# Performance work log

Hardware: AMD Instinct MI355X
Metric: run time of the kernel (lower is better)

Reference implementation:

```python
import jax, jax.numpy as jnp
import numpy as np

N = 12  # qubits; PennyLane wire 0 = most-significant bit of the state index


def _apply_ry(state, w, theta):
    # state: [B, 2^N] complex64; theta: scalar or [B]
    B = state.shape[0]
    st = state.reshape(B, 1 << w, 2, 1 << (N - 1 - w))
    h = jnp.asarray(theta) * 0.5
    c = jnp.cos(h).reshape(-1, 1, 1)
    s = jnp.sin(h).reshape(-1, 1, 1)
    a0, a1 = st[:, :, 0, :], st[:, :, 1, :]
    st = jnp.stack([c * a0 - s * a1, s * a0 + c * a1], axis=2)
    return st.reshape(B, -1)


def _apply_rz(state, w, theta):
    B = state.shape[0]
    st = state.reshape(B, 1 << w, 2, 1 << (N - 1 - w))
    ph = jnp.exp(-0.5j * jnp.asarray(theta)).reshape(-1, 1, 1)
    a0, a1 = st[:, :, 0, :], st[:, :, 1, :]
    st = jnp.stack([ph * a0, jnp.conj(ph) * a1], axis=2)
    return st.reshape(B, -1)


def _apply_cnot(state, c, t):
    B = state.shape[0]
    st = state.reshape((B,) + (2,) * N)
    ca, ta = c + 1, t + 1
    s0 = jnp.take(st, 0, axis=ca)
    s1 = jnp.take(st, 1, axis=ca)
    s1 = jnp.flip(s1, axis=ta if ta < ca else ta - 1)  # X on target when control=1
    st = jnp.stack([s0, s1], axis=ca)
    return st.reshape(B, -1)


def _rot_layer(state, ry, rz=None):
    for q in range(N):
        state = _apply_ry(state, q, ry[q])
        if rz is not None:
            state = _apply_rz(state, q, rz[q])
    return state


def _circuit(inputs, weights):
    # inputs: [B,3] (BW, COMED, dose); weights: [108] = 9 layers x 12 qubits
    B = inputs.shape[0]
    W = weights.reshape(9, N)  # l2_ry,l2_rz,l5_ry,l5_rz,l7_ry,l7_rz,l9_ry,l9_rz,l10_ry
    state = jnp.zeros((B, 1 << N), dtype=jnp.complex64).at[:, 0].set(1.0)
    for w in range(3):                      # feature encoding
        state = _apply_ry(state, w, inputs[:, w])
    state = _rot_layer(state, W[0], W[1])   # layer 2
    for c in range(3):                      # initial -> PK entanglement
        for t in range(3, 8):
            state = _apply_cnot(state, c, t)
    for c in range(3):                      # initial -> PD entanglement
        for t in range(8, 12):
            state = _apply_cnot(state, c, t)
    state = _rot_layer(state, W[2], W[3])   # layer 5
    pk = list(range(3, 8))
    for i in range(5):                      # PK ring
        state = _apply_cnot(state, pk[i], pk[(i + 1) % 5])
    pd = list(range(8, 12))
    for i in range(4):                      # PD ring
        state = _apply_cnot(state, pd[i], pd[(i + 1) % 4])
    state = _rot_layer(state, W[4], W[5])   # layer 7
    for c, t in [(3, 8), (4, 9), (5, 10), (6, 11), (7, 8)]:  # PK-PD cross
        state = _apply_cnot(state, c, t)
    state = _rot_layer(state, W[6], W[7])   # layer 9
    state = _rot_layer(state, W[8], None)   # layer 10 (RY only)
    # <Z_q> for q = 3..11
    probs = (state.real ** 2 + state.imag ** 2).reshape((B,) + (2,) * N)
    evs = []
    for q in range(3, 12):
        p = jnp.moveaxis(probs, q + 1, -1).reshape(B, -1, 2)
        evs.append(p[:, :, 0].sum(axis=1) - p[:, :, 1].sum(axis=1))
    return jnp.stack(evs, axis=1)  # [B, 9]


def _map_to_bounds(e, bounds):
    norm = (e + 1.0) * 0.5
    lo, hi = bounds[:, 0][None, :], bounds[:, 1][None, :]
    return lo + norm * (hi - lo)


def setup_inputs() -> dict:
    key = jax.random.key(0)
    k1, k2, k3, k4 = jax.random.split(key, 4)
    B = 4096
    return {
        "subject_ids": jax.random.randint(k1, (B,), 0, 1000),
        "covariates": jax.random.normal(k2, (B, 2), dtype=jnp.float32),
        "dose_intensities": jax.random.normal(k3, (B,), dtype=jnp.float32),
        "weights": jax.random.normal(k4, (108,), dtype=jnp.float32) * 0.1,
        "pk_bounds": jnp.array([[0.5, 5.0], [2.0, 20.0], [20.0, 100.0], [2.0, 30.0], [40.0, 200.0]], dtype=jnp.float32),
        "pd_bounds": jnp.array([[5.0, 25.0], [0.3, 3.0], [0.3, 0.95], [1.0, 15.0]], dtype=jnp.float32),
    }


def reference(subject_ids, covariates, dose_intensities, weights, pk_bounds, pd_bounds):
    inputs = jnp.concatenate([covariates, dose_intensities[:, None]], axis=1)  # [B,3]
    raw = _circuit(inputs, weights)
    pk_params = _map_to_bounds(raw[:, :5], pk_bounds)
    pd_params = _map_to_bounds(raw[:, 5:], pd_bounds)
    return (pk_params, pd_params)
```

## Files before the change

### kernel.cpp

```cpp
#include <hip/hip_runtime.h>


typedef float2 cplx;
__device__ inline cplx cmul(cplx a, cplx b) {
  return make_float2(a.x * b.x - a.y * b.y, a.x * b.y + a.y * b.x);
}
__device__ inline cplx cshfl_xor(cplx v, int m) {
  return make_float2(__shfl_xor(v.x, m, 64), __shfl_xor(v.y, m, 64));
}

template <int BP>
__device__ inline void rot_gate(cplx (&a)[8], float c, float s, float cz,
                                float sz) {
  if constexpr (BP < 3) {
    constexpr int m = 1 << BP;
#pragma unroll
    for (int r = 0; r < 8; r++)
      if (!(r & m)) {
        const int r1 = r | m;
        const cplx a0 = a[r], a1 = a[r1];
        const float n0x = c * a0.x - s * a1.x, n0y = c * a0.y - s * a1.y;
        const float n1x = s * a0.x + c * a1.x, n1y = s * a0.y + c * a1.y;
        a[r] = make_float2(cz * n0x + sz * n0y, cz * n0y - sz * n0x);
        a[r1] = make_float2(cz * n1x - sz * n1y, cz * n1y + sz * n1x);
      }
  } else {
    constexpr int lm = 1 << (BP - 3);
    const int bit = (threadIdx.x >> (BP - 3)) & 1;
    const float sy = bit ? s : -s;
    const float so = bit ? -sz : sz;
#pragma unroll
    for (int r = 0; r < 8; r++) {
      const cplx p = cshfl_xor(a[r], lm);
      const float nx = c * a[r].x + sy * p.x, ny = c * a[r].y + sy * p.y;
      a[r] = make_float2(cz * nx + so * ny, cz * ny - so * nx);
    }
  }
}

template <int BP>
__device__ inline void su2_gate(cplx (&a)[8], cplx u00, cplx u01, cplx u10,
                                cplx u11) {
  if constexpr (BP < 3) {
    constexpr int m = 1 << BP;
#pragma unroll
    for (int r = 0; r < 8; r++)
      if (!(r & m)) {
        const int r1 = r | m;
        const cplx a0 = a[r], a1 = a[r1];
        const cplx t0 = cmul(u00, a0), t1 = cmul(u01, a1);
        const cplx t2 = cmul(u10, a0), t3 = cmul(u11, a1);
        a[r] = make_float2(t0.x + t1.x, t0.y + t1.y);
        a[r1] = make_float2(t2.x + t3.x, t2.y + t3.y);
      }
  } else {
    constexpr int lm = 1 << (BP - 3);
    const int bit = (threadIdx.x >> (BP - 3)) & 1;
    const cplx uA = bit ? u11 : u00;
    const cplx uB = bit ? u10 : u01;
#pragma unroll
    for (int r = 0; r < 8; r++) {
      const cplx p = cshfl_xor(a[r], lm);
      const cplx t0 = cmul(uA, a[r]), t1 = cmul(uB, p);
      a[r] = make_float2(t0.x + t1.x, t0.y + t1.y);
    }
  }
}

template <int CB, int TB>
__device__ inline void cnot_rr(cplx (&a)[8]) {
#pragma unroll
  for (int r = 0; r < 8; r++)
    if ((r & (1 << CB)) && !(r & (1 << TB))) {
      const int r1 = r | (1 << TB);
      const cplx t = a[r];
      a[r] = a[r1];
      a[r1] = t;
    }
}
template <int CB, int TL>
__device__ inline void cnot_rl(cplx (&a)[8]) {
#pragma unroll
  for (int r = 0; r < 8; r++)
    if (r & (1 << CB)) a[r] = cshfl_xor(a[r], 1 << TL);
}
template <int CL, int TB>
__device__ inline void cnot_lr(cplx (&a)[8]) {
  const bool c = (threadIdx.x >> CL) & 1;
#pragma unroll
  for (int r = 0; r < 8; r++)
    if (!(r & (1 << TB))) {
      const int r1 = r | (1 << TB);
      const cplx t0 = a[r];
      a[r] = c ? a[r1] : a[r];
      a[r1] = c ? t0 : a[r1];
    }
}
template <int CL, int TL>
__device__ inline void cnot_ll(cplx (&a)[8]) {
  const bool c = (threadIdx.x >> CL) & 1;
#pragma unroll
  for (int r = 0; r < 8; r++) {
    const cplx p = cshfl_xor(a[r], 1 << TL);
    a[r] = c ? p : a[r];
  }
}

__global__ __launch_bounds__(256) void qnpe_fused(
    const float* __restrict__ cov, const float* __restrict__ dose,
    const float* __restrict__ w, const float* __restrict__ pkb,
    const float* __restrict__ pdb, float* __restrict__ out, int B) {
  __shared__ float csn[2][108];
  __shared__ cplx F[9][2];
  __shared__ cplx G[2][8];
  __shared__ cplx Ug[9][4];
  __shared__ float eS[2][9];

  const int tid = threadIdx.x;
  const int b = blockIdx.x * 256 + tid;

  float x0 = 0.f, x1 = 0.f, x2 = 0.f;
  if (b < B) {
    x0 = cov[2 * b];
    x1 = cov[2 * b + 1];
    x2 = dose[b];
  }
  const float w0 = w[0], w1 = w[1], w2 = w[2];

  if (tid < 108) {
    float s, c;
    __sincosf(0.5f * w[tid], &s, &c);
    csn[0][tid] = c;
    csn[1][tid] = s;
  }
  __syncthreads();

  if (tid < 9) {
    const float c0 = csn[0][3 + tid], s0 = csn[1][3 + tid];
    const float cz = csn[0][12 + 3 + tid], sz = csn[1][12 + 3 + tid];
    F[tid][0] = make_float2(c0 * cz, -c0 * sz);
    F[tid][1] = make_float2(s0 * cz, s0 * sz);
  } else if (tid >= 16 && tid < 25) {
    const int q = tid - 16;
    const float c6 = csn[0][6 * 12 + 3 + q], s6 = csn[1][6 * 12 + 3 + q];
    const float c7 = csn[0][7 * 12 + 3 + q], s7 = csn[1][7 * 12 + 3 + q];
    const float c8 = csn[0][8 * 12 + 3 + q], s8 = csn[1][8 * 12 + 3 + q];
    const cplx em = make_float2(c7, -s7), ep = make_float2(c7, s7);
    const cplx M00 = make_float2(c6 * em.x, c6 * em.y);
    const cplx M01 = make_float2(-s6 * em.x, -s6 * em.y);
    const cplx M10 = make_float2(s6 * ep.x, s6 * ep.y);
    const cplx M11 = make_float2(c6 * ep.x, c6 * ep.y);
    Ug[q][0] = make_float2(c8 * M00.x - s8 * M10.x, c8 * M00.y - s8 * M10.y);
    Ug[q][1] = make_float2(c8 * M01.x - s8 * M11.x, c8 * M01.y - s8 * M11.y);
    Ug[q][2] = make_float2(s8 * M00.x + c8 * M10.x, s8 * M00.y + c8 * M10.y);
    Ug[q][3] = make_float2(s8 * M01.x + c8 * M11.x, s8 * M01.y + c8 * M11.y);
  }
  __syncthreads();

  if (tid < 16) {
    const int s = tid >> 3, r = tid & 7;
    cplx g = cmul(F[6][((r >> 2) & 1) ^ s], F[7][((r >> 1) & 1) ^ s]);
    G[s][r] = cmul(g, F[8][(r & 1) ^ s]);
  }
  __syncthreads();

  const int wave = tid >> 6;
  if (wave < 2) {
    const int lane = tid & 63;
    const int s = wave;
    cplx a[8];
    cplx P = F[0][((lane >> 5) & 1) ^ s];
    P = cmul(P, F[1][((lane >> 4) & 1) ^ s]);
    P = cmul(P, F[2][((lane >> 3) & 1) ^ s]);
    P = cmul(P, F[3][((lane >> 2) & 1) ^ s]);
    P = cmul(P, F[4][((lane >> 1) & 1) ^ s]);
    P = cmul(P, F[5][(lane & 1) ^ s]);
#pragma unroll
    for (int r = 0; r < 8; r++) a[r] = cmul(P, G[s][r]);

#define ROTQ(Q, BP, LY, LZ)                                               \
  rot_gate<BP>(a, csn[0][(LY)*12 + (Q)], csn[1][(LY)*12 + (Q)],           \
               csn[0][(LZ)*12 + (Q)], csn[1][(LZ)*12 + (Q)]);
    ROTQ(3, 8, 2, 3) ROTQ(4, 7, 2, 3) ROTQ(5, 6, 2, 3)
    ROTQ(6, 5, 2, 3) ROTQ(7, 4, 2, 3) ROTQ(8, 3, 2, 3)
    ROTQ(9, 2, 2, 3) ROTQ(10, 1, 2, 3) ROTQ(11, 0, 2, 3)
    cnot_ll<5, 4>(a);
    cnot_ll<4, 3>(a);
    cnot_ll<3, 2>(a);
    cnot_ll<2, 1>(a);
    cnot_ll<1, 5>(a);
    cnot_lr<0, 2>(a);
    cnot_rr<2, 1>(a);
    cnot_rr<1, 0>(a);
    cnot_rl<0, 0>(a);
    ROTQ(3, 8, 4, 5) ROTQ(4, 7, 4, 5) ROTQ(5, 6, 4, 5)
    ROTQ(6, 5, 4, 5) ROTQ(7, 4, 4, 5) ROTQ(8, 3, 4, 5)
    ROTQ(9, 2, 4, 5) ROTQ(10, 1, 4, 5) ROTQ(11, 0, 4, 5)
#undef ROTQ
    cnot_ll<5, 0>(a);
    cnot_lr<4, 2>(a);
    cnot_lr<3, 1>(a);
    cnot_lr<2, 0>(a);
    cnot_ll<1, 0>(a);
    su2_gate<8>(a, Ug[0][0], Ug[0][1], Ug[0][2], Ug[0][3]);
    su2_gate<7>(a, Ug[1][0], Ug[1][1], Ug[1][2], Ug[1][3]);
    su2_gate<6>(a, Ug[2][0], Ug[2][1], Ug[2][2], Ug[2][3]);
    su2_gate<5>(a, Ug[3][0], Ug[3][1], Ug[3][2], Ug[3][3]);
    su2_gate<4>(a, Ug[4][0], Ug[4][1], Ug[4][2], Ug[4][3]);
    su2_gate<3>(a, Ug[5][0], Ug[5][1], Ug[5][2], Ug[5][3]);
    su2_gate<2>(a, Ug[6][0], Ug[6][1], Ug[6][2], Ug[6][3]);
    su2_gate<1>(a, Ug[7][0], Ug[7][1], Ug[7][2], Ug[7][3]);
    su2_gate<0>(a, Ug[8][0], Ug[8][1], Ug[8][2], Ug[8][3]);

    float p[8], tot = 0.f;
#pragma unroll
    for (int r = 0; r < 8; r++) {
      p[r] = a[r].x * a[r].x + a[r].y * a[r].y;
      tot += p[r];
    }
    float v = tot;
#pragma unroll
    for (int k = 0; k < 6; k++) {
      const float pr = __shfl_xor(v, 1 << k, 64);
      v = ((lane >> k) & 1) ? (pr - v) : (v + pr);
    }
    if (lane == 32) eS[s][0] = v;
    if (lane == 16) eS[s][1] = v;
    if (lane == 8) eS[s][2] = v;
    if (lane == 4) eS[s][3] = v;
    if (lane == 2) eS[s][4] = v;
    if (lane == 1) eS[s][5] = v;
    float v6 = 0.f, v7 = 0.f, v8 = 0.f;
#pragma unroll
    for (int r = 0; r < 8; r++) {
      v6 += ((r >> 2) & 1) ? -p[r] : p[r];
      v7 += ((r >> 1) & 1) ? -p[r] : p[r];
      v8 += (r & 1) ? -p[r] : p[r];
    }
#pragma unroll
    for (int off = 1; off < 64; off <<= 1) {
      v6 += __shfl_xor(v6, off, 64);
      v7 += __shfl_xor(v7, off, 64);
      v8 += __shfl_xor(v8, off, 64);
    }
    if (lane == 0) {
      eS[s][6] = v6;
      eS[s][7] = v7;
      eS[s][8] = v8;
    }
  }
  __syncthreads();

  if (b >= B) return;
  const float g = __cosf(x0 + w0) * __cosf(x1 + w1) * __cosf(x2 + w2);
  const float podd = 0.5f * (1.f - g);

#pragma unroll
  for (int q = 0; q < 9; q++) {
    const float e = eS[0][q] + (eS[1][q] - eS[0][q]) * podd;
    const float norm = 0.5f * (e + 1.f);
    if (q < 5) {
      out[b * 5 + q] = pkb[2 * q] + norm * (pkb[2 * q + 1] - pkb[2 * q]);
    } else {
      const int j = q - 5;
      out[B * 5 + b * 4 + j] =
          pdb[2 * j] + norm * (pdb[2 * j + 1] - pdb[2 * j]);
    }
  }
}

extern "C" void kernel_launch(void* const* d_in, const int* in_sizes, int n_in,
                              void* d_out, int out_size, void* d_ws,
                              size_t ws_size, hipStream_t stream) {
  const float* cov = (const float*)d_in[1];
  const float* dose = (const float*)d_in[2];
  const float* wts = (const float*)d_in[3];
  const float* pkb = (const float*)d_in[4];
  const float* pdb = (const float*)d_in[5];
  float* out = (float*)d_out;
  const int B = in_sizes[2];

  hipLaunchKernelGGL(qnpe_fused, dim3((B + 255) / 256), dim3(256), 0, stream,
                     cov, dose, wts, pkb, pdb, out, B);
}
```

Baseline: 71.00 us.

## Simulate both branch states redundantly in every wave, dropping final barrier

Each wave now simulates both the even and odd parity statevectors in registers, instead of waves 0 and 1 each handling one while the other two waves idle. The 9 expectation values are then broadcast within the wave via shuffles rather than through shared memory, which removes the final __syncthreads. The cost is four times the redundant gate arithmetic per block and higher register pressure from holding two 8-amplitude arrays. In exchange the block no longer serializes on two waves before the output phase.

```diff
diff --git a/kernel.cpp b/kernel.cpp
--- a/kernel.cpp
+++ b/kernel.cpp
@@ -10,19 +10,28 @@
 }
 
 template <int BP>
-__device__ inline void rot_gate(cplx (&a)[8], float c, float s, float cz,
-                                float sz) {
+__device__ inline void rot_gate(cplx (&A)[8], cplx (&D)[8], float c, float s,
+                                float cz, float sz) {
   if constexpr (BP < 3) {
     constexpr int m = 1 << BP;
 #pragma unroll
     for (int r = 0; r < 8; r++)
       if (!(r & m)) {
         const int r1 = r | m;
-        const cplx a0 = a[r], a1 = a[r1];
-        const float n0x = c * a0.x - s * a1.x, n0y = c * a0.y - s * a1.y;
-        const float n1x = s * a0.x + c * a1.x, n1y = s * a0.y + c * a1.y;
-        a[r] = make_float2(cz * n0x + sz * n0y, cz * n0y - sz * n0x);
-        a[r1] = make_float2(cz * n1x - sz * n1y, cz * n1y + sz * n1x);
+        {
+          const cplx a0 = A[r], a1 = A[r1];
+          const float n0x = c * a0.x - s * a1.x, n0y = c * a0.y - s * a1.y;
+          const float n1x = s * a0.x + c * a1.x, n1y = s * a0.y + c * a1.y;
+          A[r] = make_float2(cz * n0x + sz * n0y, cz * n0y - sz * n0x);
+          A[r1] = make_float2(cz * n1x - sz * n1y, cz * n1y + sz * n1x);
+        }
+        {
+          const cplx a0 = D[r], a1 = D[r1];
+          const float n0x = c * a0.x - s * a1.x, n0y = c * a0.y - s * a1.y;
+          const float n1x = s * a0.x + c * a1.x, n1y = s * a0.y + c * a1.y;
+          D[r] = make_float2(cz * n0x + sz * n0y, cz * n0y - sz * n0x);
+          D[r1] = make_float2(cz * n1x - sz * n1y, cz * n1y + sz * n1x);
+        }
       }
   } else {
     constexpr int lm = 1 << (BP - 3);
@@ -31,27 +40,39 @@
     const float so = bit ? -sz : sz;
 #pragma unroll
     for (int r = 0; r < 8; r++) {
-      const cplx p = cshfl_xor(a[r], lm);
-      const float nx = c * a[r].x + sy * p.x, ny = c * a[r].y + sy * p.y;
-      a[r] = make_float2(cz * nx + so * ny, cz * ny - so * nx);
+      const cplx pA = cshfl_xor(A[r], lm);
+      const cplx pD = cshfl_xor(D[r], lm);
+      const float nxA = c * A[r].x + sy * pA.x, nyA = c * A[r].y + sy * pA.y;
+      A[r] = make_float2(cz * nxA + so * nyA, cz * nyA - so * nxA);
+      const float nxD = c * D[r].x + sy * pD.x, nyD = c * D[r].y + sy * pD.y;
+      D[r] = make_float2(cz * nxD + so * nyD, cz * nyD - so * nxD);
     }
   }
 }
 
 template <int BP>
-__device__ inline void su2_gate(cplx (&a)[8], cplx u00, cplx u01, cplx u10,
-                                cplx u11) {
+__device__ inline void su2_gate(cplx (&A)[8], cplx (&D)[8], cplx u00, cplx u01,
+                                cplx u10, cplx u11) {
   if constexpr (BP < 3) {
     constexpr int m = 1 << BP;
 #pragma unroll
     for (int r = 0; r < 8; r++)
       if (!(r & m)) {
         const int r1 = r | m;
-        const cplx a0 = a[r], a1 = a[r1];
-        const cplx t0 = cmul(u00, a0), t1 = cmul(u01, a1);
-        const cplx t2 = cmul(u10, a0), t3 = cmul(u11, a1);
-        a[r] = make_float2(t0.x + t1.x, t0.y + t1.y);
-        a[r1] = make_float2(t2.x + t3.x, t2.y + t3.y);
+        {
+          const cplx a0 = A[r], a1 = A[r1];
+          const cplx t0 = cmul(u00, a0), t1 = cmul(u01, a1);
+          const cplx t2 = cmul(u10, a0), t3 = cmul(u11, a1);
+          A[r] = make_float2(t0.x + t1.x, t0.y + t1.y);
+          A[r1] = make_float2(t2.x + t3.x, t2.y + t3.y);
+        }
+        {
+          const cplx a0 = D[r], a1 = D[r1];
+          const cplx t0 = cmul(u00, a0), t1 = cmul(u01, a1);
+          const cplx t2 = cmul(u10, a0), t3 = cmul(u11, a1);
+          D[r] = make_float2(t0.x + t1.x, t0.y + t1.y);
+          D[r1] = make_float2(t2.x + t3.x, t2.y + t3.y);
+        }
       }
   } else {
     constexpr int lm = 1 << (BP - 3);
@@ -60,49 +81,71 @@
     const cplx uB = bit ? u10 : u01;
 #pragma unroll
     for (int r = 0; r < 8; r++) {
-      const cplx p = cshfl_xor(a[r], lm);
-      const cplx t0 = cmul(uA, a[r]), t1 = cmul(uB, p);
-      a[r] = make_float2(t0.x + t1.x, t0.y + t1.y);
+      const cplx pA = cshfl_xor(A[r], lm);
+      const cplx pD = cshfl_xor(D[r], lm);
+      {
+        const cplx t0 = cmul(uA, A[r]), t1 = cmul(uB, pA);
+        A[r] = make_float2(t0.x + t1.x, t0.y + t1.y);
+      }
+      {
+        const cplx t0 = cmul(uA, D[r]), t1 = cmul(uB, pD);
+        D[r] = make_float2(t0.x + t1.x, t0.y + t1.y);
+      }
     }
   }
 }
 
 template <int CB, int TB>
-__device__ inline void cnot_rr(cplx (&a)[8]) {
+__device__ inline void cnot_rr(cplx (&A)[8], cplx (&D)[8]) {
 #pragma unroll
   for (int r = 0; r < 8; r++)
     if ((r & (1 << CB)) && !(r & (1 << TB))) {
       const int r1 = r | (1 << TB);
-      const cplx t = a[r];
-      a[r] = a[r1];
-      a[r1] = t;
+      const cplx tA = A[r];
+      A[r] = A[r1];
+      A[r1] = tA;
+      const cplx tD = D[r];
+      D[r] = D[r1];
+      D[r1] = tD;
     }
 }
 template <int CB, int TL>
-__device__ inline void cnot_rl(cplx (&a)[8]) {
+__device__ inline void cnot_rl(cplx (&A)[8], cplx (&D)[8]) {
 #pragma unroll
   for (int r = 0; r < 8; r++)
-    if (r & (1 << CB)) a[r] = cshfl_xor(a[r], 1 << TL);
+    if (r & (1 << CB)) {
+      A[r] = cshfl_xor(A[r], 1 << TL);
+      D[r] = cshfl_xor(D[r], 1 << TL);
+    }
 }
 template <int CL, int TB>
-__device__ inline void cnot_lr(cplx (&a)[8]) {
+__device__ inline void cnot_lr(cplx (&A)[8], cplx (&D)[8]) {
   const bool c = (threadIdx.x >> CL) & 1;
 #pragma unroll
   for (int r = 0; r < 8; r++)
     if (!(r & (1 << TB))) {
       const int r1 = r | (1 << TB);
-      const cplx t0 = a[r];
-      a[r] = c ? a[r1] : a[r];
-      a[r1] = c ? t0 : a[r1];
+      {
+        const cplx t0 = A[r];
+        A[r] = c ? A[r1] : A[r];
+        A[r1] = c ? t0 : A[r1];
+      }
+      {
+        const cplx t0 = D[r];
+        D[r] = c ? D[r1] : D[r];
+        D[r1] = c ? t0 : D[r1];
+      }
     }
 }
 template <int CL, int TL>
-__device__ inline void cnot_ll(cplx (&a)[8]) {
+__device__ inline void cnot_ll(cplx (&A)[8], cplx (&D)[8]) {
   const bool c = (threadIdx.x >> CL) & 1;
 #pragma unroll
   for (int r = 0; r < 8; r++) {
-    const cplx p = cshfl_xor(a[r], 1 << TL);
-    a[r] = c ? p : a[r];
+    const cplx pA = cshfl_xor(A[r], 1 << TL);
+    A[r] = c ? pA : A[r];
+    const cplx pD = cshfl_xor(D[r], 1 << TL);
+    D[r] = c ? pD : D[r];
   }
 }
 
@@ -114,7 +157,6 @@
   __shared__ cplx F[9][2];
   __shared__ cplx G[2][8];
   __shared__ cplx Ug[9][4];
-  __shared__ float eS[2][9];
 
   const int tid = threadIdx.x;
   const int b = blockIdx.x * 256 + tid;
@@ -164,92 +206,118 @@
   }
   __syncthreads();
 
-  const int wave = tid >> 6;
-  if (wave < 2) {
-    const int lane = tid & 63;
-    const int s = wave;
-    cplx a[8];
-    cplx P = F[0][((lane >> 5) & 1) ^ s];
-    P = cmul(P, F[1][((lane >> 4) & 1) ^ s]);
-    P = cmul(P, F[2][((lane >> 3) & 1) ^ s]);
-    P = cmul(P, F[3][((lane >> 2) & 1) ^ s]);
-    P = cmul(P, F[4][((lane >> 1) & 1) ^ s]);
-    P = cmul(P, F[5][(lane & 1) ^ s]);
-#pragma unroll
-    for (int r = 0; r < 8; r++) a[r] = cmul(P, G[s][r]);
-
-#define ROTQ(Q, BP, LY, LZ)                                               \
-  rot_gate<BP>(a, csn[0][(LY)*12 + (Q)], csn[1][(LY)*12 + (Q)],           \
+  const int lane = tid & 63;
+  cplx a0s[8], a1s[8];
+  {
+    cplx P0 = F[0][(lane >> 5) & 1];
+    cplx P1 = F[0][((lane >> 5) & 1) ^ 1];
+    P0 = cmul(P0, F[1][(lane >> 4) & 1]);
+    P1 = cmul(P1, F[1][((lane >> 4) & 1) ^ 1]);
+    P0 = cmul(P0, F[2][(lane >> 3) & 1]);
+    P1 = cmul(P1, F[2][((lane >> 3) & 1) ^ 1]);
+    P0 = cmul(P0, F[3][(lane >> 2) & 1]);
+    P1 = cmul(P1, F[3][((lane >> 2) & 1) ^ 1]);
+    P0 = cmul(P0, F[4][(lane >> 1) & 1]);
+    P1 = cmul(P1, F[4][((lane >> 1) & 1) ^ 1]);
+    P0 = cmul(P0, F[5][lane & 1]);
+    P1 = cmul(P1, F[5][(lane & 1) ^ 1]);
+#pragma unroll
+    for (int r = 0; r < 8; r++) {
+      a0s[r] = cmul(P0, G[0][r]);
+      a1s[r] = cmul(P1, G[1][r]);
+    }
+  }
+
+#define ROTQ(Q, BP, LY, LZ)                                                \
+  rot_gate<BP>(a0s, a1s, csn[0][(LY)*12 + (Q)], csn[1][(LY)*12 + (Q)],     \
                csn[0][(LZ)*12 + (Q)], csn[1][(LZ)*12 + (Q)]);
-    ROTQ(3, 8, 2, 3) ROTQ(4, 7, 2, 3) ROTQ(5, 6, 2, 3)
-    ROTQ(6, 5, 2, 3) ROTQ(7, 4, 2, 3) ROTQ(8, 3, 2, 3)
-    ROTQ(9, 2, 2, 3) ROTQ(10, 1, 2, 3) ROTQ(11, 0, 2, 3)
-    cnot_ll<5, 4>(a);
-    cnot_ll<4, 3>(a);
-    cnot_ll<3, 2>(a);
-    cnot_ll<2, 1>(a);
-    cnot_ll<1, 5>(a);
-    cnot_lr<0, 2>(a);
-    cnot_rr<2, 1>(a);
-    cnot_rr<1, 0>(a);
-    cnot_rl<0, 0>(a);
-    ROTQ(3, 8, 4, 5) ROTQ(4, 7, 4, 5) ROTQ(5, 6, 4, 5)
-    ROTQ(6, 5, 4, 5) ROTQ(7, 4, 4, 5) ROTQ(8, 3, 4, 5)
-    ROTQ(9, 2, 4, 5) ROTQ(10, 1, 4, 5) ROTQ(11, 0, 4, 5)
+  ROTQ(3, 8, 2, 3) ROTQ(4, 7, 2, 3) ROTQ(5, 6, 2, 3)
+  ROTQ(6, 5, 2, 3) ROTQ(7, 4, 2, 3) ROTQ(8, 3, 2, 3)
+  ROTQ(9, 2, 2, 3) ROTQ(10, 1, 2, 3) ROTQ(11, 0, 2, 3)
+  cnot_ll<5, 4>(a0s, a1s);
+  cnot_ll<4, 3>(a0s, a1s);
+  cnot_ll<3, 2>(a0s, a1s);
+  cnot_ll<2, 1>(a0s, a1s);
+  cnot_ll<1, 5>(a0s, a1s);
+  cnot_lr<0, 2>(a0s, a1s);
+  cnot_rr<2, 1>(a0s, a1s);
+  cnot_rr<1, 0>(a0s, a1s);
+  cnot_rl<0, 0>(a0s, a1s);
+  ROTQ(3, 8, 4, 5) ROTQ(4, 7, 4, 5) ROTQ(5, 6, 4, 5)
+  ROTQ(6, 5, 4, 5) ROTQ(7, 4, 4, 5) ROTQ(8, 3, 4, 5)
+  ROTQ(9, 2, 4, 5) ROTQ(10, 1, 4, 5) ROTQ(11, 0, 4, 5)
 #undef ROTQ
-    cnot_ll<5, 0>(a);
-    cnot_lr<4, 2>(a);
-    cnot_lr<3, 1>(a);
-    cnot_lr<2, 0>(a);
-    cnot_ll<1, 0>(a);
-    su2_gate<8>(a, Ug[0][0], Ug[0][1], Ug[0][2], Ug[0][3]);
-    su2_gate<7>(a, Ug[1][0], Ug[1][1], Ug[1][2], Ug[1][3]);
-    su2_gate<6>(a, Ug[2][0], Ug[2][1], Ug[2][2], Ug[2][3]);
-    su2_gate<5>(a, Ug[3][0], Ug[3][1], Ug[3][2], Ug[3][3]);
-    su2_gate<4>(a, Ug[4][0], Ug[4][1], Ug[4][2], Ug[4][3]);
-    su2_gate<3>(a, Ug[5][0], Ug[5][1], Ug[5][2], Ug[5][3]);
-    su2_gate<2>(a, Ug[6][0], Ug[6][1], Ug[6][2], Ug[6][3]);
-    su2_gate<1>(a, Ug[7][0], Ug[7][1], Ug[7][2], Ug[7][3]);
-    su2_gate<0>(a, Ug[8][0], Ug[8][1], Ug[8][2], Ug[8][3]);
-
-    float p[8], tot = 0.f;
-#pragma unroll
-    for (int r = 0; r < 8; r++) {
-      p[r] = a[r].x * a[r].x + a[r].y * a[r].y;
-      tot += p[r];
-    }
-    float v = tot;
-#pragma unroll
-    for (int k = 0; k < 6; k++) {
-      const float pr = __shfl_xor(v, 1 << k, 64);
-      v = ((lane >> k) & 1) ? (pr - v) : (v + pr);
-    }
-    if (lane == 32) eS[s][0] = v;
-    if (lane == 16) eS[s][1] = v;
-    if (lane == 8) eS[s][2] = v;
-    if (lane == 4) eS[s][3] = v;
-    if (lane == 2) eS[s][4] = v;
-    if (lane == 1) eS[s][5] = v;
-    float v6 = 0.f, v7 = 0.f, v8 = 0.f;
-#pragma unroll
-    for (int r = 0; r < 8; r++) {
-      v6 += ((r >> 2) & 1) ? -p[r] : p[r];
-      v7 += ((r >> 1) & 1) ? -p[r] : p[r];
-      v8 += (r & 1) ? -p[r] : p[r];
-    }
-#pragma unroll
-    for (int off = 1; off < 64; off <<= 1) {
-      v6 += __shfl_xor(v6, off, 64);
-      v7 += __shfl_xor(v7, off, 64);
-      v8 += __shfl_xor(v8, off, 64);
-    }
-    if (lane == 0) {
-      eS[s][6] = v6;
-      eS[s][7] = v7;
-      eS[s][8] = v8;
-    }
-  }
-  __syncthreads();
+  cnot_ll<5, 0>(a0s, a1s);
+  cnot_lr<4, 2>(a0s, a1s);
+  cnot_lr<3, 1>(a0s, a1s);
+  cnot_lr<2, 0>(a0s, a1s);
+  cnot_ll<1, 0>(a0s, a1s);
+  su2_gate<8>(a0s, a1s, Ug[0][0], Ug[0][1], Ug[0][2], Ug[0][3]);
+  su2_gate<7>(a0s, a1s, Ug[1][0], Ug[1][1], Ug[1][2], Ug[1][3]);
+  su2_gate<6>(a0s, a1s, Ug[2][0], Ug[2][1], Ug[2][2], Ug[2][3]);
+  su2_gate<5>(a0s, a1s, Ug[3][0], Ug[3][1], Ug[3][2], Ug[3][3]);
+  su2_gate<4>(a0s, a1s, Ug[4][0], Ug[4][1], Ug[4][2], Ug[4][3]);
+  su2_gate<3>(a0s, a1s, Ug[5][0], Ug[5][1], Ug[5][2], Ug[5][3]);
+  su2_gate<2>(a0s, a1s, Ug[6][0], Ug[6][1], Ug[6][2], Ug[6][3]);
+  su2_gate<1>(a0s, a1s, Ug[7][0], Ug[7][1], Ug[7][2], Ug[7][3]);
+  su2_gate<0>(a0s, a1s, Ug[8][0], Ug[8][1], Ug[8][2], Ug[8][3]);
+
+  float4 m0, m1;
+  {
+    float p0[8], p1[8];
+    float t0 = 0.f, t1 = 0.f;
+#pragma unroll
+    for (int r = 0; r < 8; r++) {
+      p0[r] = a0s[r].x * a0s[r].x + a0s[r].y * a0s[r].y;
+      t0 += p0[r];
+      p1[r] = a1s[r].x * a1s[r].x + a1s[r].y * a1s[r].y;
+      t1 += p1[r];
+    }
+    float v60 = 0.f, v70 = 0.f, v80 = 0.f, v61 = 0.f, v71 = 0.f, v81 = 0.f;
+#pragma unroll
+    for (int r = 0; r < 8; r++) {
+      v60 += ((r >> 2) & 1) ? -p0[r] : p0[r];
+      v70 += ((r >> 1) & 1) ? -p0[r] : p0[r];
+      v80 += (r & 1) ? -p0[r] : p0[r];
+      v61 += ((r >> 2) & 1) ? -p1[r] : p1[r];
+      v71 += ((r >> 1) & 1) ? -p1[r] : p1[r];
+      v81 += (r & 1) ? -p1[r] : p1[r];
+    }
+    m0 = make_float4(t0, v60, v70, v80);
+    m1 = make_float4(t1, v61, v71, v81);
+  }
+#pragma unroll
+  for (int k = 0; k < 6; k++) {
+    const int msk = 1 << k;
+    const float q0x = __shfl_xor(m0.x, msk, 64);
+    const float q0y = __shfl_xor(m0.y, msk, 64);
+    const float q0z = __shfl_xor(m0.z, msk, 64);
+    const float q0w = __shfl_xor(m0.w, msk, 64);
+    const float q1x = __shfl_xor(m1.x, msk, 64);
+    const float q1y = __shfl_xor(m1.y, msk, 64);
+    const float q1z = __shfl_xor(m1.z, msk, 64);
+    const float q1w = __shfl_xor(m1.w, msk, 64);
+    const bool hi = (lane >> k) & 1;
+    m0.x = hi ? (q0x - m0.x) : (m0.x + q0x);
+    m0.y = hi ? (q0y - m0.y) : (m0.y + q0y);
+    m0.z = hi ? (q0z - m0.z) : (m0.z + q0z);
+    m0.w = hi ? (q0w - m0.w) : (m0.w + q0w);
+    m1.x = hi ? (q1x - m1.x) : (m1.x + q1x);
+    m1.y = hi ? (q1y - m1.y) : (m1.y + q1y);
+    m1.z = hi ? (q1z - m1.z) : (m1.z + q1z);
+    m1.w = hi ? (q1w - m1.w) : (m1.w + q1w);
+  }
+
+  const float E0[9] = {__shfl(m0.x, 32, 64), __shfl(m0.x, 16, 64),
+                       __shfl(m0.x, 8, 64),  __shfl(m0.x, 4, 64),
+                       __shfl(m0.x, 2, 64),  __shfl(m0.x, 1, 64),
+                       __shfl(m0.y, 0, 64),  __shfl(m0.z, 0, 64),
+                       __shfl(m0.w, 0, 64)};
+  const float E1[9] = {__shfl(m1.x, 32, 64), __shfl(m1.x, 16, 64),
+                       __shfl(m1.x, 8, 64),  __shfl(m1.x, 4, 64),
+                       __shfl(m1.x, 2, 64),  __shfl(m1.x, 1, 64),
+                       __shfl(m1.y, 0, 64),  __shfl(m1.z, 0, 64),
+                       __shfl(m1.w, 0, 64)};
 
   if (b >= B) return;
   const float g = __cosf(x0 + w0) * __cosf(x1 + w1) * __cosf(x2 + w2);
@@ -257,7 +325,7 @@
 
 #pragma unroll
   for (int q = 0; q < 9; q++) {
-    const float e = eS[0][q] + (eS[1][q] - eS[0][q]) * podd;
+    const float e = E0[q] + (E1[q] - E0[q]) * podd;
     const float norm = 0.5f * (e + 1.f);
     if (q < 5) {
       out[b * 5 + q] = pkb[2 * q] + norm * (pkb[2 * q + 1] - pkb[2 * q]);
```

New measurement: 78.18 us. 10.1% more time.
